# Optimization experiments

Measured on AMD Instinct MI355X. Metric: run time of the kernel, lower is better.

Reference implementation:

```python
import jax, jax.numpy as jnp
import numpy as np
import math

D_MODEL = 1024
N_HEADS = 16
D_HEAD = D_MODEL // N_HEADS
EPS = 1e-5


def layer_norm(x, w, b):
    mu = jnp.mean(x, axis=-1, keepdims=True)
    var = jnp.mean(jnp.square(x - mu), axis=-1, keepdims=True)
    return (x - mu) * jax.lax.rsqrt(var + EPS) * w + b


def setup_inputs() -> dict:
    key = jax.random.key(0)
    ks = jax.random.split(key, 8)
    b, n, d = 1, 4096, D_MODEL
    s = 0.02
    return {
        "x": jax.random.normal(ks[0], (b, n, d), dtype=jnp.float32),
        "ln1_w": jnp.ones((d,), jnp.float32),
        "ln1_b": jnp.zeros((d,), jnp.float32),
        "ln2_w": jnp.ones((d,), jnp.float32),
        "ln2_b": jnp.zeros((d,), jnp.float32),
        "w_qkv": jax.random.normal(ks[1], (d, 3 * d), jnp.float32) * s,  # [in, out]
        "w_o": jax.random.normal(ks[2], (d, d), jnp.float32) * s,
        "w_ff1": jax.random.normal(ks[3], (d, 4 * d), jnp.float32) * s,
        "b_ff1": jnp.zeros((4 * d,), jnp.float32),
        "w_ff2": jax.random.normal(ks[4], (4 * d, d), jnp.float32) * s,
        "b_ff2": jnp.zeros((d,), jnp.float32),
    }


def reference(x, ln1_w, ln1_b, ln2_w, ln2_b, w_qkv, w_o, w_ff1, b_ff1, w_ff2, b_ff2):
    b, n, d = x.shape
    # --- attention sub-block ---
    h = layer_norm(x, ln1_w, ln1_b)
    qkv = (h @ w_qkv).reshape(b, n, 3, N_HEADS, D_HEAD)
    q, k, v = qkv[:, :, 0], qkv[:, :, 1], qkv[:, :, 2]  # [b, n, h, dh]
    scale = 1.0 / math.sqrt(D_HEAD)
    s = jnp.einsum("bqhd,bkhd->bhqk", q, k) * scale  # materialized [b,h,n,n]
    causal = jnp.tril(jnp.ones((n, n), dtype=bool))
    s = jnp.where(causal, s, -jnp.inf)
    a = jax.nn.softmax(s, axis=-1)
    out = jnp.einsum("bhqk,bkhd->bqhd", a, v).reshape(b, n, d)
    x = x + out @ w_o
    # --- FFN sub-block ---
    h2 = layer_norm(x, ln2_w, ln2_b)
    ff = jax.nn.gelu(h2 @ w_ff1 + b_ff1, approximate=False) @ w_ff2 + b_ff2
    return x + ff
```

## Files before the change

kernel.cpp:

```cpp
#include <hip/hip_runtime.h>
#include <hip/hip_bf16.h>
#include <cstdint>
#include <cstddef>

typedef __attribute__((ext_vector_type(8))) __bf16 bf16x8;
typedef __attribute__((ext_vector_type(4))) __bf16 bf16x4;
typedef __attribute__((ext_vector_type(4))) float f32x4;
typedef __attribute__((ext_vector_type(16))) float f32x16;
typedef __attribute__((ext_vector_type(4))) unsigned int uint4v;

#define MFMA16(a, b, c) __builtin_amdgcn_mfma_f32_16x16x32_bf16(a, b, c, 0, 0, 0)
#define MFMA32(a, b, c) __builtin_amdgcn_mfma_f32_32x32x16_bf16(a, b, c, 0, 0, 0)

__device__ __forceinline__ void gload_lds16(const void* g, void* l) {
  __builtin_amdgcn_global_load_lds(
      (__attribute__((address_space(1))) uint32_t*)g,
      (__attribute__((address_space(3))) uint32_t*)l,
      16, 0, 0);
}

__device__ __forceinline__ unsigned pkbf(float a, float b) {
  unsigned short x = __builtin_bit_cast(unsigned short, (__bf16)a);
  unsigned short y = __builtin_bit_cast(unsigned short, (__bf16)b);
  return (unsigned)x | ((unsigned)y << 16);
}

__global__ __launch_bounds__(256) void transpose_all_kernel(
    const float* __restrict__ w_qkv, __bf16* __restrict__ wqkvT,
    const float* __restrict__ w_o, __bf16* __restrict__ woT,
    const float* __restrict__ w_ff1, __bf16* __restrict__ wff1T,
    const float* __restrict__ w_ff2, __bf16* __restrict__ wff2T) {
  __shared__ float tile[32][33];
  int bid = blockIdx.x;
  const float* in; __bf16* out; int K, N, bx, by;
  if (bid < 3072)      { in = w_qkv; out = wqkvT; K = 1024; N = 3072; bx = bid % 96;  by = bid / 96; }
  else if (bid < 4096) { int b = bid - 3072; in = w_o;   out = woT;   K = 1024; N = 1024; bx = b % 32;  by = b / 32; }
  else if (bid < 8192) { int b = bid - 4096; in = w_ff1; out = wff1T; K = 1024; N = 4096; bx = b % 128; by = b / 128; }
  else                 { int b = bid - 8192; in = w_ff2; out = wff2T; K = 4096; N = 1024; bx = b % 32;  by = b / 32; }
  int tx = threadIdx.x, ty = threadIdx.y;
  int gcol = bx * 32 + tx;
#pragma unroll
  for (int j = 0; j < 4; j++) {
    int grow = by * 32 + ty + j * 8;
    tile[ty + j * 8][tx] = in[(size_t)grow * N + gcol];
  }
  __syncthreads();
#pragma unroll
  for (int j = 0; j < 4; j++) {
    int n = bx * 32 + ty + j * 8;
    out[(size_t)n * K + by * 32 + tx] = (__bf16)tile[tx][ty + j * 8];
  }
}

__global__ __launch_bounds__(256) void ln_kernel(
    const float* __restrict__ x, const float* __restrict__ w,
    const float* __restrict__ b, __bf16* __restrict__ out) {
  int row = blockIdx.x;
  int t = threadIdx.x;
  const float4* xr = (const float4*)(x + (size_t)row * 1024);
  float4 v = xr[t];
  float s = v.x + v.y + v.z + v.w;
  float sq = v.x * v.x + v.y * v.y + v.z * v.z + v.w * v.w;
#pragma unroll
  for (int m = 1; m < 64; m <<= 1) {
    s += __shfl_xor(s, m);
    sq += __shfl_xor(sq, m);
  }
  __shared__ float rs[4], rq[4];
  int wid = t >> 6;
  if ((t & 63) == 0) { rs[wid] = s; rq[wid] = sq; }
  __syncthreads();
  s = rs[0] + rs[1] + rs[2] + rs[3];
  sq = rq[0] + rq[1] + rq[2] + rq[3];
  float mean = s * (1.0f / 1024.0f);
  float var = sq * (1.0f / 1024.0f) - mean * mean;
  float rstd = rsqrtf(var + 1e-5f);
  int c = t * 4;
  float4 wv = ((const float4*)w)[t];
  float4 bv = ((const float4*)b)[t];
  bf16x4 o;
  o[0] = (__bf16)((v.x - mean) * rstd * wv.x + bv.x);
  o[1] = (__bf16)((v.y - mean) * rstd * wv.y + bv.y);
  o[2] = (__bf16)((v.z - mean) * rstd * wv.z + bv.z);
  o[3] = (__bf16)((v.w - mean) * rstd * wv.w + bv.w);
  *(bf16x4*)(out + (size_t)row * 1024 + c) = o;
}

template <int EPI>
__global__ __launch_bounds__(256, 2) void gemm_kernel(
    const __bf16* __restrict__ A, const __bf16* __restrict__ BT,
    int M, int N, int K,
    const float* __restrict__ resid, const float* __restrict__ bias,
    float* __restrict__ outf, __bf16* __restrict__ outb) {
  __shared__ __bf16 lsA[128 * 64];
  __shared__ __bf16 lsB[128 * 64];
  int t = threadIdx.x;
  int m0 = blockIdx.y * 128, n0 = blockIdx.x * 128;
  int wid = t >> 6, lane = t & 63, lo = lane & 15, g = lane >> 4;
  int wr = wid >> 1, wc = wid & 1;
  f32x4 acc[4][4] = {};
  const __bf16* ag = A + (size_t)(m0 + (t >> 3)) * K + (t & 7) * 8;
  const __bf16* bg = BT + (size_t)(n0 + (t >> 3)) * K + (t & 7) * 8;
  for (int k0 = 0; k0 < K; k0 += 64) {
#pragma unroll
    for (int i = 0; i < 4; i++) {
      gload_lds16(ag + (size_t)i * 32 * K + k0, &lsA[i * 2048 + t * 8]);
      gload_lds16(bg + (size_t)i * 32 * K + k0, &lsB[i * 2048 + t * 8]);
    }
    __syncthreads();
#pragma unroll
    for (int kk = 0; kk < 2; kk++) {
      bf16x8 af[4], bfr[4];
#pragma unroll
      for (int mi = 0; mi < 4; mi++)
        af[mi] = *(const bf16x8*)&lsA[(wr * 64 + mi * 16 + lo) * 64 + kk * 32 + g * 8];
#pragma unroll
      for (int ni = 0; ni < 4; ni++)
        bfr[ni] = *(const bf16x8*)&lsB[(wc * 64 + ni * 16 + lo) * 64 + kk * 32 + g * 8];
#pragma unroll
      for (int mi = 0; mi < 4; mi++)
#pragma unroll
        for (int ni = 0; ni < 4; ni++)
          acc[mi][ni] = MFMA16(af[mi], bfr[ni], acc[mi][ni]);
    }
    __syncthreads();
  }
#pragma unroll
  for (int mi = 0; mi < 4; mi++) {
#pragma unroll
    for (int ni = 0; ni < 4; ni++) {
      int col = n0 + wc * 64 + ni * 16 + lo;
      int row0 = m0 + wr * 64 + mi * 16 + g * 4;
#pragma unroll
      for (int r = 0; r < 4; r++) {
        int row = row0 + r;
        float val = acc[mi][ni][r];
        size_t idx = (size_t)row * N + col;
        outf[idx] = resid[idx] + val;
      }
    }
  }
}

template <int EPI>
__global__ __launch_bounds__(512, 2) void gemm256_kernel(
    const __bf16* __restrict__ A, const __bf16* __restrict__ BT,
    int M, int N, int K, int nkc,
    const float* __restrict__ bias, __bf16* __restrict__ outb,
    __bf16* __restrict__ P0, __bf16* __restrict__ P1,
    __bf16* __restrict__ P2, __bf16* __restrict__ P3) {
  __shared__ __bf16 lsA[2][2][128 * 64];
  __shared__ __bf16 lsB[2][2][128 * 64];
  int nbx = N >> 8;
  int nwg = (M >> 8) * nbx;
  int bid = blockIdx.x;
  int swz = (bid & 7) * (nwg >> 3) + (bid >> 3);
  int m0 = (swz / nbx) << 8, n0 = (swz % nbx) << 8;
  int kc = blockIdx.y;
  int kt0 = kc * nkc;
  int t = threadIdx.x;
  int wid = t >> 6, lane = t & 63, lo = lane & 15, g = lane >> 4;
  int wm = wid >> 2, wn = wid & 3;
  int srow = t >> 3, sgrp = t & 7;

  auto stA = [&](int d, int h, int kt) {
#pragma unroll
    for (int i = 0; i < 2; i++) {
      int row = i * 64 + srow;
      int gs = (sgrp ^ (row & 7)) * 8;
      gload_lds16(A + (size_t)(m0 + h * 128 + row) * K + kt * 64 + gs,
                  &lsA[d][h][(i * 512 + t) * 8]);
    }
  };
  auto stB = [&](int d, int h, int kt) {
#pragma unroll
    for (int i = 0; i < 2; i++) {
      int row = i * 64 + srow;
      int gs = (sgrp ^ (row & 7)) * 8;
      gload_lds16(BT + (size_t)(n0 + h * 128 + row) * K + kt * 64 + gs,
                  &lsB[d][h][(i * 512 + t) * 8]);
    }
  };
  auto rdA = [&](int d, int f, int kk) -> bf16x8 {
    int row = (f & 3) * 32 + wm * 16 + lo;
    return *(const bf16x8*)&lsA[d][f >> 2][row * 64 + (((kk * 4 + g) ^ (lo & 7)) * 8)];
  };
  auto rdB = [&](int d, int ni, int kk) -> bf16x8 {
    int row = (ni & 1) * 64 + wn * 16 + lo;
    return *(const bf16x8*)&lsB[d][ni >> 1][row * 64 + (((kk * 4 + g) ^ (lo & 7)) * 8)];
  };

  f32x4 acc[8][4] = {};
  stA(0, 0, kt0); stB(0, 0, kt0); stB(0, 1, kt0); stA(0, 1, kt0);
  asm volatile("s_waitcnt vmcnt(4)" ::: "memory");
  __builtin_amdgcn_s_barrier();

  for (int ki = 0; ki < nkc; ki++) {
    int kt = kt0 + ki;
    int d = ki & 1, nx = d ^ 1;
    bool pf = (ki + 1) < nkc;
    bf16x8 fa[4][2], fb0[2][2], fb1[2][2];
#pragma unroll
    for (int f = 0; f < 4; f++) { fa[f][0] = rdA(d, f, 0); fa[f][1] = rdA(d, f, 1); }
#pragma unroll
    for (int n = 0; n < 2; n++) { fb0[n][0] = rdB(d, n, 0); fb0[n][1] = rdB(d, n, 1); }
    if (pf) { stA(nx, 0, kt + 1); stB(nx, 0, kt + 1); }
    __builtin_amdgcn_s_barrier();
    __builtin_amdgcn_s_setprio(1);
#pragma unroll
    for (int f = 0; f < 4; f++)
#pragma unroll
      for (int n = 0; n < 2; n++) {
        acc[f][n] = MFMA16(fa[f][0], fb0[n][0], acc[f][n]);
        acc[f][n] = MFMA16(fa[f][1], fb0[n][1], acc[f][n]);
      }
    __builtin_amdgcn_s_setprio(0);
    asm volatile("s_waitcnt vmcnt(6)" ::: "memory");
    __builtin_amdgcn_s_barrier();
#pragma unroll
    for (int n = 0; n < 2; n++) { fb1[n][0] = rdB(d, 2 + n, 0); fb1[n][1] = rdB(d, 2 + n, 1); }
    if (pf) stB(nx, 1, kt + 1);
    __builtin_amdgcn_s_barrier();
    __builtin_amdgcn_s_setprio(1);
#pragma unroll
    for (int f = 0; f < 4; f++)
#pragma unroll
      for (int n = 0; n < 2; n++) {
        acc[f][2 + n] = MFMA16(fa[f][0], fb1[n][0], acc[f][2 + n]);
        acc[f][2 + n] = MFMA16(fa[f][1], fb1[n][1], acc[f][2 + n]);
      }
    __builtin_amdgcn_s_setprio(0);
    asm volatile("s_waitcnt vmcnt(6)" ::: "memory");
    __builtin_amdgcn_s_barrier();
#pragma unroll
    for (int f = 0; f < 4; f++) { fa[f][0] = rdA(d, 4 + f, 0); fa[f][1] = rdA(d, 4 + f, 1); }
    if (pf) stA(nx, 1, kt + 1);
    __builtin_amdgcn_s_barrier();
    __builtin_amdgcn_s_setprio(1);
#pragma unroll
    for (int f = 0; f < 4; f++)
#pragma unroll
      for (int n = 0; n < 2; n++) {
        acc[4 + f][2 + n] = MFMA16(fa[f][0], fb1[n][0], acc[4 + f][2 + n]);
        acc[4 + f][2 + n] = MFMA16(fa[f][1], fb1[n][1], acc[4 + f][2 + n]);
      }
    __builtin_amdgcn_s_setprio(0);
    __builtin_amdgcn_s_barrier();
    __builtin_amdgcn_s_setprio(1);
#pragma unroll
    for (int f = 0; f < 4; f++)
#pragma unroll
      for (int n = 0; n < 2; n++) {
        acc[4 + f][n] = MFMA16(fa[f][0], fb0[n][0], acc[4 + f][n]);
        acc[4 + f][n] = MFMA16(fa[f][1], fb0[n][1], acc[4 + f][n]);
      }
    __builtin_amdgcn_s_setprio(0);
    asm volatile("s_waitcnt vmcnt(4)" ::: "memory");
    __builtin_amdgcn_s_barrier();
  }

  __bf16* pk = (EPI == 4) ? ((kc == 0) ? P0 : (kc == 1) ? P1 : (kc == 2) ? P2 : P3)
                          : nullptr;
#pragma unroll
  for (int f = 0; f < 8; f++) {
    int row0 = m0 + (f >> 2) * 128 + (f & 3) * 32 + wm * 16 + g * 4;
#pragma unroll
    for (int ni = 0; ni < 4; ni++) {
      int col = n0 + (ni >> 1) * 128 + (ni & 1) * 64 + wn * 16 + lo;
      if (EPI == 0) {
        int sE = col >> 10, rem = col & 1023, hh = rem >> 6, dd = rem & 63;
        if (sE < 2) {
          float qs = (sE == 0) ? 0.1803368801111204f : 1.0f;
#pragma unroll
          for (int r = 0; r < 4; r++)
            outb[((size_t)(sE * 16 + hh) * 4096 + row0 + r) * 64 + dd] =
                (__bf16)(acc[f][ni][r] * qs);
        } else {
          bf16x4 pk4;
#pragma unroll
          for (int r = 0; r < 4; r++) pk4[r] = (__bf16)acc[f][ni][r];
          *(bf16x4*)&outb[(size_t)32 * 4096 * 64 + ((size_t)(hh * 64 + dd)) * 4096 + row0] = pk4;
        }
      } else if (EPI == 2) {
        float bv = bias[col];
#pragma unroll
        for (int r = 0; r < 4; r++) {
          float vv = acc[f][ni][r] + bv;
          float gg = 0.5f * vv * (1.0f + erff(vv * 0.70710678118f));
          outb[(size_t)(row0 + r) * N + col] = (__bf16)gg;
        }
      } else {
#pragma unroll
        for (int r = 0; r < 4; r++)
          pk[(size_t)(row0 + r) * N + col] = (__bf16)acc[f][ni][r];
      }
    }
  }
}

__global__ __launch_bounds__(256) void ff2_reduce_kernel(
    const __bf16* __restrict__ p0, const __bf16* __restrict__ p1,
    const __bf16* __restrict__ p2, const __bf16* __restrict__ p3,
    const float* __restrict__ x2, const float* __restrict__ bias,
    float* __restrict__ out) {
  size_t i8 = ((size_t)blockIdx.x * 256 + threadIdx.x) * 8;
  bf16x8 a = *(const bf16x8*)&p0[i8];
  bf16x8 b = *(const bf16x8*)&p1[i8];
  bf16x8 c = *(const bf16x8*)&p2[i8];
  bf16x8 d = *(const bf16x8*)&p3[i8];
  int col = (int)(i8 & 1023);
  float4 xa = *(const float4*)&x2[i8];
  float4 xb = *(const float4*)&x2[i8 + 4];
  float4 ba = *(const float4*)&bias[col];
  float4 bb = *(const float4*)&bias[col + 4];
  float4 oa, ob;
  oa.x = xa.x + ba.x + (float)a[0] + (float)b[0] + (float)c[0] + (float)d[0];
  oa.y = xa.y + ba.y + (float)a[1] + (float)b[1] + (float)c[1] + (float)d[1];
  oa.z = xa.z + ba.z + (float)a[2] + (float)b[2] + (float)c[2] + (float)d[2];
  oa.w = xa.w + ba.w + (float)a[3] + (float)b[3] + (float)c[3] + (float)d[3];
  ob.x = xb.x + bb.x + (float)a[4] + (float)b[4] + (float)c[4] + (float)d[4];
  ob.y = xb.y + bb.y + (float)a[5] + (float)b[5] + (float)c[5] + (float)d[5];
  ob.z = xb.z + bb.z + (float)a[6] + (float)b[6] + (float)c[6] + (float)d[6];
  ob.w = xb.w + bb.w + (float)a[7] + (float)b[7] + (float)c[7] + (float)d[7];
  *(float4*)&out[i8] = oa;
  *(float4*)&out[i8 + 4] = ob;
}

__global__ __launch_bounds__(512, 4) void attn_kernel(
    const __bf16* __restrict__ Q, const __bf16* __restrict__ Kb,
    const __bf16* __restrict__ VTb, __bf16* __restrict__ O) {
  constexpr int NSEQ = 4096;
  __shared__ __bf16 lds[2][2][2][64 * 64];
  int orig = blockIdx.x;
  int xcd = orig & 7, rank = orig >> 3;
  int hv = rank >> 5;
  int hd2 = (rank >> 4) & 1;
  int itr = rank & 15;
  int head = xcd * 2 + hd2;
  int it = hv ? itr : (31 - itr);
  int t = threadIdx.x, wid = t >> 6, lane = t & 63;
  int lo = lane & 31, hi = lane >> 5;
  int qsub = wid & 3, kpar = wid >> 2;
  const __bf16* kh = Kb + (size_t)head * NSEQ * 64;
  const __bf16* vth = VTb + (size_t)head * 64 * NSEQ;
  int qlow = it * 128 + qsub * 32;
  int qrow = qlow + lo;
  const __bf16* qh = Q + (size_t)head * NSEQ * 64 + (size_t)qrow * 64;
  bf16x8 bq[4];
#pragma unroll
  for (int c = 0; c < 4; c++) bq[c] = *(const bf16x8*)(qh + c * 16 + hi * 8);

  const unsigned onesu = 0x3F803F80u;
  uint4v onev = {onesu, onesu, onesu, onesu};
  bf16x8 vones = __builtin_bit_cast(bf16x8, onev);

  f32x16 acc0 = {}, acc1 = {};
  f32x16 lacc = {};
  int srow = t >> 3;
  int sgs = ((t & 7) ^ (srow & 7)) * 8;

  auto stage_tile = [&](int d, int par, int kt) {
    gload_lds16(kh + (size_t)(kt * 64 + srow) * 64 + sgs, &lds[d][par][0][t * 8]);
    gload_lds16(vth + (size_t)srow * NSEQ + kt * 64 + sgs, &lds[d][par][1][t * 8]);
  };

  int ns = it + 1;
  stage_tile(0, 0, 0);
  stage_tile(0, 1, 1);
  __syncthreads();
  for (int j = 0; j < ns; j++) {
    int cur = j & 1;
    if (j + 1 < ns) {
      stage_tile(cur ^ 1, 0, 2 * j + 2);
      stage_tile(cur ^ 1, 1, 2 * j + 3);
    }
    int kt = 2 * j + kpar;
    if (kt * 64 <= qlow + 31) {
      const __bf16* lk = lds[cur][kpar][0];
      const __bf16* lvt = lds[cur][kpar][1];
      f32x16 s0 = {}, s1 = {};
      __builtin_amdgcn_s_setprio(1);
#pragma unroll
      for (int c = 0; c < 4; c++) {
        bf16x8 ka0 = *(const bf16x8*)&lk[(size_t)lo * 64 + (((c * 2 + hi) ^ (lo & 7)) * 8)];
        bf16x8 ka1 = *(const bf16x8*)&lk[(size_t)(32 + lo) * 64 + (((c * 2 + hi) ^ (lo & 7)) * 8)];
        s0 = MFMA32(ka0, bq[c], s0);
        s1 = MFMA32(ka1, bq[c], s1);
      }
      __builtin_amdgcn_s_setprio(0);
      if (kt * 64 + 63 > qlow) {
#pragma unroll
        for (int i = 0; i < 16; i++) {
          int key0 = kt * 64 + (i & 3) + 8 * (i >> 2) + 4 * hi;
          if (key0 > qrow) s0[i] = -3.0e38f;
          if (key0 + 32 > qrow) s1[i] = -3.0e38f;
        }
      }
#pragma unroll
      for (int i = 0; i < 16; i++) {
        s0[i] = exp2f(s0[i]);
        s1[i] = exp2f(s1[i]);
      }
      uint4v pw[4];
#pragma unroll
      for (int b = 0; b < 2; b++) {
        int off = b * 8;
        unsigned a0 = pkbf(s0[off + 0], s0[off + 1]);
        unsigned a1 = pkbf(s0[off + 2], s0[off + 3]);
        unsigned b0 = pkbf(s0[off + 4], s0[off + 5]);
        unsigned b1 = pkbf(s0[off + 6], s0[off + 7]);
        asm("v_permlane32_swap_b32 %0, %1" : "+v"(a0), "+v"(b0));
        asm("v_permlane32_swap_b32 %0, %1" : "+v"(a1), "+v"(b1));
        pw[b][0] = a0; pw[b][1] = a1; pw[b][2] = b0; pw[b][3] = b1;
        unsigned c0 = pkbf(s1[off + 0], s1[off + 1]);
        unsigned c1 = pkbf(s1[off + 2], s1[off + 3]);
        unsigned d0 = pkbf(s1[off + 4], s1[off + 5]);
        unsigned d1 = pkbf(s1[off + 6], s1[off + 7]);
        asm("v_permlane32_swap_b32 %0, %1" : "+v"(c0), "+v"(d0));
        asm("v_permlane32_swap_b32 %0, %1" : "+v"(c1), "+v"(d1));
        pw[2 + b][0] = c0; pw[2 + b][1] = c1; pw[2 + b][2] = d0; pw[2 + b][3] = d1;
      }
      __builtin_amdgcn_s_setprio(1);
#pragma unroll
      for (int b = 0; b < 4; b++) {
        bf16x8 pf = __builtin_bit_cast(bf16x8, pw[b]);
        bf16x8 va0 = *(const bf16x8*)&lvt[(size_t)lo * 64 + (((b * 2 + hi) ^ (lo & 7)) * 8)];
        bf16x8 va1 = *(const bf16x8*)&lvt[(size_t)(32 + lo) * 64 + (((b * 2 + hi) ^ (lo & 7)) * 8)];
        acc0 = MFMA32(va0, pf, acc0);
        acc1 = MFMA32(va1, pf, acc1);
        lacc = MFMA32(vones, pf, lacc);
      }
      __builtin_amdgcn_s_setprio(0);
    }
    __syncthreads();
  }
  float* fl = (float*)lds;
  float* lbuf = fl;
  float* ab = fl + 256;
  __bf16* bounce = (__bf16*)(fl + 256 + 9216);
  if (kpar == 1) {
    lbuf[qsub * 64 + lane] = lacc[0];
    int base = (qsub * 64 + lane) * 36;
#pragma unroll
    for (int k2 = 0; k2 < 16; k2 += 4) {
      float4 v0; v0.x = acc0[k2]; v0.y = acc0[k2 + 1]; v0.z = acc0[k2 + 2]; v0.w = acc0[k2 + 3];
      *(float4*)&ab[base + k2] = v0;
      float4 v1; v1.x = acc1[k2]; v1.y = acc1[k2 + 1]; v1.z = acc1[k2 + 2]; v1.w = acc1[k2 + 3];
      *(float4*)&ab[base + 16 + k2] = v1;
    }
  }
  __syncthreads();
  if (kpar == 0) {
    float lsum = lacc[0] + lbuf[qsub * 64 + lane];
    float linv = 1.0f / lsum;
    int base = (qsub * 64 + lane) * 36;
    f32x16 b0, b1;
#pragma unroll
    for (int k2 = 0; k2 < 16; k2 += 4) {
      float4 v0 = *(float4*)&ab[base + k2];
      b0[k2] = v0.x; b0[k2 + 1] = v0.y; b0[k2 + 2] = v0.z; b0[k2 + 3] = v0.w;
      float4 v1 = *(float4*)&ab[base + 16 + k2];
      b1[k2] = v1.x; b1[k2 + 1] = v1.y; b1[k2 + 2] = v1.z; b1[k2 + 3] = v1.w;
    }
    __bf16* region = bounce + qsub * 2048;
#pragma unroll
    for (int dt = 0; dt < 2; dt++) {
#pragma unroll
      for (int rp = 0; rp < 8; rp++) {
        int r = rp * 2;
        float a0 = dt ? acc1[r] : acc0[r], a1 = dt ? acc1[r + 1] : acc0[r + 1];
        float c0 = dt ? b1[r] : b0[r], c1 = dt ? b1[r + 1] : b0[r + 1];
        float e0 = (a0 + c0) * linv;
        float e1 = (a1 + c1) * linv;
        int d = dt * 32 + (r & 3) + 8 * (r >> 2) + 4 * hi;
        int bytecol = d * 2;
        int g16 = bytecol >> 4, rem16 = bytecol & 15;
        *(unsigned*)((char*)region + lo * 128 + ((g16 ^ (lo & 7)) * 16 + rem16)) = pkbf(e0, e1);
      }
    }
#pragma unroll
    for (int j2 = 0; j2 < 4; j2++) {
      int idx = j2 * 64 + lane;
      int row = idx >> 3, g = idx & 7;
      bf16x8 v = *(const bf16x8*)((char*)region + row * 128 + ((g ^ (row & 7)) * 16));
      *(bf16x8*)&O[(size_t)(it * 128 + qsub * 32 + row) * 1024 + head * 64 + g * 8] = v;
    }
  }
}

extern "C" void kernel_launch(void* const* d_in, const int* in_sizes, int n_in,
                              void* d_out, int out_size, void* d_ws, size_t ws_size,
                              hipStream_t stream) {
  const float* x = (const float*)d_in[0];
  const float* ln1_w = (const float*)d_in[1];
  const float* ln1_b = (const float*)d_in[2];
  const float* ln2_w = (const float*)d_in[3];
  const float* ln2_b = (const float*)d_in[4];
  const float* w_qkv = (const float*)d_in[5];
  const float* w_o = (const float*)d_in[6];
  const float* w_ff1 = (const float*)d_in[7];
  const float* b_ff1 = (const float*)d_in[8];
  const float* w_ff2 = (const float*)d_in[9];
  const float* b_ff2 = (const float*)d_in[10];
  float* out = (float*)d_out;

  const size_t D = 1024, NT = 4096;
  __bf16* wqkvT = (__bf16*)d_ws;
  __bf16* woT = wqkvT + 3072 * D;
  __bf16* wff1T = woT + D * D;
  __bf16* wff2T = wff1T + 4096 * D;
  __bf16* hbuf = wff2T + D * 4096;
  __bf16* qkvb = hbuf + NT * D;
  __bf16* attnb = qkvb + 3 * NT * D;
  __bf16* a1 = qkvb;
  float* x2 = (float*)(attnb + NT * D);
  __bf16* p0 = (__bf16*)d_ws;
  __bf16* p1 = p0 + NT * D;
  __bf16* p2 = hbuf;
  __bf16* p3 = (__bf16*)(x2 + NT * D);

  dim3 tb(32, 8);
  transpose_all_kernel<<<12288, tb, 0, stream>>>(w_qkv, wqkvT, w_o, woT,
                                                 w_ff1, wff1T, w_ff2, wff2T);

  ln_kernel<<<4096, 256, 0, stream>>>(x, ln1_w, ln1_b, hbuf);
  gemm256_kernel<0><<<192, 512, 0, stream>>>(hbuf, wqkvT, 4096, 3072, 1024, 16,
                                             nullptr, qkvb, nullptr, nullptr, nullptr, nullptr);
  attn_kernel<<<512, 512, 0, stream>>>(
      qkvb, qkvb + 16 * NT * 64, qkvb + 32 * NT * 64, attnb);
  gemm_kernel<1><<<dim3(1024 / 128, 4096 / 128), 256, 0, stream>>>(
      attnb, woT, 4096, 1024, 1024, x, nullptr, x2, nullptr);
  ln_kernel<<<4096, 256, 0, stream>>>(x2, ln2_w, ln2_b, hbuf);
  gemm256_kernel<2><<<256, 512, 0, stream>>>(hbuf, wff1T, 4096, 4096, 1024, 16,
                                             b_ff1, a1, nullptr, nullptr, nullptr, nullptr);
  gemm256_kernel<4><<<dim3(64, 4), 512, 0, stream>>>(a1, wff2T, 4096, 1024, 4096, 16,
                                                     nullptr, nullptr, p0, p1, p2, p3);
  ff2_reduce_kernel<<<2048, 256, 0, stream>>>(p0, p1, p2, p3, x2, b_ff2, out);
}
```

Before: 247.8 us.

## Split-K the output projection, fuse residual with LN2, single-buffer attention LDS

The output-projection GEMM is split into two K-halves that write bf16 partials, so it launches twice as many workgroups. A new kernel sums the partials with the residual and applies LayerNorm 2, replacing the separate GEMM epilogue and ln_kernel pass. The attention kernel drops the double-buffered K/V staging for a single buffer loaded synchronously each iteration and stages the kpar=1 partial output as bf16, which cuts LDS use and raises the occupancy hint to 6. The trade-offs are lost prefetch overlap in attention, extra bf16 rounding of the partial sums, and an extra partial-buffer round trip through memory.

```diff
diff --git a/kernel.cpp b/kernel.cpp
--- a/kernel.cpp
+++ b/kernel.cpp
@@ -86,22 +86,21 @@
   *(bf16x4*)(out + (size_t)row * 1024 + c) = o;
 }
 
-template <int EPI>
-__global__ __launch_bounds__(256, 2) void gemm_kernel(
+__global__ __launch_bounds__(256, 2) void gemm_splitk128_kernel(
     const __bf16* __restrict__ A, const __bf16* __restrict__ BT,
-    int M, int N, int K,
-    const float* __restrict__ resid, const float* __restrict__ bias,
-    float* __restrict__ outf, __bf16* __restrict__ outb) {
+    int M, int N, int K, int kchunk, __bf16* __restrict__ P) {
   __shared__ __bf16 lsA[128 * 64];
   __shared__ __bf16 lsB[128 * 64];
   int t = threadIdx.x;
   int m0 = blockIdx.y * 128, n0 = blockIdx.x * 128;
+  int kbase = blockIdx.z * kchunk;
+  __bf16* pout = P + (size_t)blockIdx.z * M * N;
   int wid = t >> 6, lane = t & 63, lo = lane & 15, g = lane >> 4;
   int wr = wid >> 1, wc = wid & 1;
   f32x4 acc[4][4] = {};
   const __bf16* ag = A + (size_t)(m0 + (t >> 3)) * K + (t & 7) * 8;
   const __bf16* bg = BT + (size_t)(n0 + (t >> 3)) * K + (t & 7) * 8;
-  for (int k0 = 0; k0 < K; k0 += 64) {
+  for (int k0 = kbase; k0 < kbase + kchunk; k0 += 64) {
 #pragma unroll
     for (int i = 0; i < 4; i++) {
       gload_lds16(ag + (size_t)i * 32 * K + k0, &lsA[i * 2048 + t * 8]);
@@ -132,14 +131,52 @@
       int col = n0 + wc * 64 + ni * 16 + lo;
       int row0 = m0 + wr * 64 + mi * 16 + g * 4;
 #pragma unroll
-      for (int r = 0; r < 4; r++) {
-        int row = row0 + r;
-        float val = acc[mi][ni][r];
-        size_t idx = (size_t)row * N + col;
-        outf[idx] = resid[idx] + val;
-      }
-    }
-  }
+      for (int r = 0; r < 4; r++)
+        pout[(size_t)(row0 + r) * N + col] = (__bf16)acc[mi][ni][r];
+    }
+  }
+}
+
+__global__ __launch_bounds__(256) void out_reduce_ln_kernel(
+    const __bf16* __restrict__ p0, const __bf16* __restrict__ p1,
+    const float* __restrict__ x, const float* __restrict__ w,
+    const float* __restrict__ b, float* __restrict__ x2,
+    __bf16* __restrict__ h) {
+  int row = blockIdx.x, t = threadIdx.x;
+  size_t base = (size_t)row * 1024 + t * 4;
+  bf16x4 a = *(const bf16x4*)&p0[base];
+  bf16x4 b4 = *(const bf16x4*)&p1[base];
+  float4 xv = *(const float4*)&x[base];
+  float4 v;
+  v.x = xv.x + (float)a[0] + (float)b4[0];
+  v.y = xv.y + (float)a[1] + (float)b4[1];
+  v.z = xv.z + (float)a[2] + (float)b4[2];
+  v.w = xv.w + (float)a[3] + (float)b4[3];
+  *(float4*)&x2[base] = v;
+  float s = v.x + v.y + v.z + v.w;
+  float sq = v.x * v.x + v.y * v.y + v.z * v.z + v.w * v.w;
+#pragma unroll
+  for (int m = 1; m < 64; m <<= 1) {
+    s += __shfl_xor(s, m);
+    sq += __shfl_xor(sq, m);
+  }
+  __shared__ float rs[4], rq[4];
+  int wid = t >> 6;
+  if ((t & 63) == 0) { rs[wid] = s; rq[wid] = sq; }
+  __syncthreads();
+  s = rs[0] + rs[1] + rs[2] + rs[3];
+  sq = rq[0] + rq[1] + rq[2] + rq[3];
+  float mean = s * (1.0f / 1024.0f);
+  float var = sq * (1.0f / 1024.0f) - mean * mean;
+  float rstd = rsqrtf(var + 1e-5f);
+  float4 wv = ((const float4*)w)[t];
+  float4 bv = ((const float4*)b)[t];
+  bf16x4 o;
+  o[0] = (__bf16)((v.x - mean) * rstd * wv.x + bv.x);
+  o[1] = (__bf16)((v.y - mean) * rstd * wv.y + bv.y);
+  o[2] = (__bf16)((v.z - mean) * rstd * wv.z + bv.z);
+  o[3] = (__bf16)((v.w - mean) * rstd * wv.w + bv.w);
+  *(bf16x4*)&h[base] = o;
 }
 
 template <int EPI>
@@ -326,11 +363,11 @@
   *(float4*)&out[i8 + 4] = ob;
 }
 
-__global__ __launch_bounds__(512, 4) void attn_kernel(
+__global__ __launch_bounds__(512, 6) void attn_kernel(
     const __bf16* __restrict__ Q, const __bf16* __restrict__ Kb,
     const __bf16* __restrict__ VTb, __bf16* __restrict__ O) {
   constexpr int NSEQ = 4096;
-  __shared__ __bf16 lds[2][2][2][64 * 64];
+  __shared__ __bf16 lds[2][2][64 * 64];
   int orig = blockIdx.x;
   int xcd = orig & 7, rank = orig >> 3;
   int hv = rank >> 5;
@@ -345,6 +382,7 @@
   const __bf16* vth = VTb + (size_t)head * 64 * NSEQ;
   int qlow = it * 128 + qsub * 32;
   int qrow = qlow + lo;
+  int lastk = (qlow + 31) >> 6;
   const __bf16* qh = Q + (size_t)head * NSEQ * 64 + (size_t)qrow * 64;
   bf16x8 bq[4];
 #pragma unroll
@@ -359,31 +397,30 @@
   int srow = t >> 3;
   int sgs = ((t & 7) ^ (srow & 7)) * 8;
 
-  auto stage_tile = [&](int d, int par, int kt) {
-    gload_lds16(kh + (size_t)(kt * 64 + srow) * 64 + sgs, &lds[d][par][0][t * 8]);
-    gload_lds16(vth + (size_t)srow * NSEQ + kt * 64 + sgs, &lds[d][par][1][t * 8]);
-  };
-
-  int ns = it + 1;
-  stage_tile(0, 0, 0);
-  stage_tile(0, 1, 1);
-  __syncthreads();
-  for (int j = 0; j < ns; j++) {
-    int cur = j & 1;
-    if (j + 1 < ns) {
-      stage_tile(cur ^ 1, 0, 2 * j + 2);
-      stage_tile(cur ^ 1, 1, 2 * j + 3);
-    }
-    int kt = 2 * j + kpar;
-    if (kt * 64 <= qlow + 31) {
-      const __bf16* lk = lds[cur][kpar][0];
-      const __bf16* lvt = lds[cur][kpar][1];
+  int off[4];
+#pragma unroll
+  for (int c = 0; c < 4; c++) off[c] = lo * 64 + (((c * 2 + hi) ^ (lo & 7)) * 8);
+  const __bf16* lk = &lds[kpar][0][0];
+  const __bf16* lvt = &lds[kpar][1][0];
+  const __bf16* khs = kh + srow * 64 + sgs;
+  const __bf16* vts = vth + (size_t)srow * NSEQ + sgs;
+
+  int ns2 = it + 1;
+  for (int j = 0; j < ns2; j++) {
+    int k0 = 2 * j;
+    gload_lds16(khs + (size_t)k0 * 4096, &lds[0][0][t * 8]);
+    gload_lds16(vts + k0 * 64, &lds[0][1][t * 8]);
+    gload_lds16(khs + (size_t)(k0 + 1) * 4096, &lds[1][0][t * 8]);
+    gload_lds16(vts + (k0 + 1) * 64, &lds[1][1][t * 8]);
+    __syncthreads();
+    int kt = k0 + kpar;
+    if (kt <= lastk) {
       f32x16 s0 = {}, s1 = {};
       __builtin_amdgcn_s_setprio(1);
 #pragma unroll
       for (int c = 0; c < 4; c++) {
-        bf16x8 ka0 = *(const bf16x8*)&lk[(size_t)lo * 64 + (((c * 2 + hi) ^ (lo & 7)) * 8)];
-        bf16x8 ka1 = *(const bf16x8*)&lk[(size_t)(32 + lo) * 64 + (((c * 2 + hi) ^ (lo & 7)) * 8)];
+        bf16x8 ka0 = *(const bf16x8*)&lk[off[c]];
+        bf16x8 ka1 = *(const bf16x8*)&lk[2048 + off[c]];
         s0 = MFMA32(ka0, bq[c], s0);
         s1 = MFMA32(ka1, bq[c], s1);
       }
@@ -404,28 +441,29 @@
       uint4v pw[4];
 #pragma unroll
       for (int b = 0; b < 2; b++) {
-        int off = b * 8;
-        unsigned a0 = pkbf(s0[off + 0], s0[off + 1]);
-        unsigned a1 = pkbf(s0[off + 2], s0[off + 3]);
-        unsigned b0 = pkbf(s0[off + 4], s0[off + 5]);
-        unsigned b1 = pkbf(s0[off + 6], s0[off + 7]);
+        int off2 = b * 8;
+        unsigned a0 = pkbf(s0[off2 + 0], s0[off2 + 1]);
+        unsigned a1 = pkbf(s0[off2 + 2], s0[off2 + 3]);
+        unsigned b0 = pkbf(s0[off2 + 4], s0[off2 + 5]);
+        unsigned b1 = pkbf(s0[off2 + 6], s0[off2 + 7]);
         asm("v_permlane32_swap_b32 %0, %1" : "+v"(a0), "+v"(b0));
         asm("v_permlane32_swap_b32 %0, %1" : "+v"(a1), "+v"(b1));
         pw[b][0] = a0; pw[b][1] = a1; pw[b][2] = b0; pw[b][3] = b1;
-        unsigned c0 = pkbf(s1[off + 0], s1[off + 1]);
-        unsigned c1 = pkbf(s1[off + 2], s1[off + 3]);
-        unsigned d0 = pkbf(s1[off + 4], s1[off + 5]);
-        unsigned d1 = pkbf(s1[off + 6], s1[off + 7]);
+        unsigned c0 = pkbf(s1[off2 + 0], s1[off2 + 1]);
+        unsigned c1 = pkbf(s1[off2 + 2], s1[off2 + 3]);
+        unsigned d0 = pkbf(s1[off2 + 4], s1[off2 + 5]);
+        unsigned d1 = pkbf(s1[off2 + 6], s1[off2 + 7]);
         asm("v_permlane32_swap_b32 %0, %1" : "+v"(c0), "+v"(d0));
         asm("v_permlane32_swap_b32 %0, %1" : "+v"(c1), "+v"(d1));
-        pw[2 + b][0] = c0; pw[2 + b][1] = c1; pw[2 + b][2] = d0; pw[2 + b][3] = d1;
+        pw[2 + b][0] = c0; pw[2 + b][1] = c1; pw[2 + b][2] = d0;
+        pw[2 + b][3] = d1;
       }
       __builtin_amdgcn_s_setprio(1);
 #pragma unroll
       for (int b = 0; b < 4; b++) {
         bf16x8 pf = __builtin_bit_cast(bf16x8, pw[b]);
-        bf16x8 va0 = *(const bf16x8*)&lvt[(size_t)lo * 64 + (((b * 2 + hi) ^ (lo & 7)) * 8)];
-        bf16x8 va1 = *(const bf16x8*)&lvt[(size_t)(32 + lo) * 64 + (((b * 2 + hi) ^ (lo & 7)) * 8)];
+        bf16x8 va0 = *(const bf16x8*)&lvt[off[b]];
+        bf16x8 va1 = *(const bf16x8*)&lvt[2048 + off[b]];
         acc0 = MFMA32(va0, pf, acc0);
         acc1 = MFMA32(va1, pf, acc1);
         lacc = MFMA32(vones, pf, lacc);
@@ -434,48 +472,45 @@
     }
     __syncthreads();
   }
+
   float* fl = (float*)lds;
   float* lbuf = fl;
-  float* ab = fl + 256;
-  __bf16* bounce = (__bf16*)(fl + 256 + 9216);
+  __bf16* bounce = (__bf16*)(fl + 256);
+  __bf16* region = bounce + qsub * 2048;
   if (kpar == 1) {
     lbuf[qsub * 64 + lane] = lacc[0];
-    int base = (qsub * 64 + lane) * 36;
-#pragma unroll
-    for (int k2 = 0; k2 < 16; k2 += 4) {
-      float4 v0; v0.x = acc0[k2]; v0.y = acc0[k2 + 1]; v0.z = acc0[k2 + 2]; v0.w = acc0[k2 + 3];
-      *(float4*)&ab[base + k2] = v0;
-      float4 v1; v1.x = acc1[k2]; v1.y = acc1[k2 + 1]; v1.z = acc1[k2 + 2]; v1.w = acc1[k2 + 3];
-      *(float4*)&ab[base + 16 + k2] = v1;
-    }
-  }
-  __syncthreads();
-  if (kpar == 0) {
-    float lsum = lacc[0] + lbuf[qsub * 64 + lane];
-    float linv = 1.0f / lsum;
-    int base = (qsub * 64 + lane) * 36;
-    f32x16 b0, b1;
-#pragma unroll
-    for (int k2 = 0; k2 < 16; k2 += 4) {
-      float4 v0 = *(float4*)&ab[base + k2];
-      b0[k2] = v0.x; b0[k2 + 1] = v0.y; b0[k2 + 2] = v0.z; b0[k2 + 3] = v0.w;
-      float4 v1 = *(float4*)&ab[base + 16 + k2];
-      b1[k2] = v1.x; b1[k2 + 1] = v1.y; b1[k2 + 2] = v1.z; b1[k2 + 3] = v1.w;
-    }
-    __bf16* region = bounce + qsub * 2048;
 #pragma unroll
     for (int dt = 0; dt < 2; dt++) {
 #pragma unroll
       for (int rp = 0; rp < 8; rp++) {
         int r = rp * 2;
-        float a0 = dt ? acc1[r] : acc0[r], a1 = dt ? acc1[r + 1] : acc0[r + 1];
-        float c0 = dt ? b1[r] : b0[r], c1 = dt ? b1[r + 1] : b0[r + 1];
-        float e0 = (a0 + c0) * linv;
-        float e1 = (a1 + c1) * linv;
+        float e0 = dt ? acc1[r] : acc0[r];
+        float e1 = dt ? acc1[r + 1] : acc0[r + 1];
         int d = dt * 32 + (r & 3) + 8 * (r >> 2) + 4 * hi;
         int bytecol = d * 2;
         int g16 = bytecol >> 4, rem16 = bytecol & 15;
         *(unsigned*)((char*)region + lo * 128 + ((g16 ^ (lo & 7)) * 16 + rem16)) = pkbf(e0, e1);
+      }
+    }
+  }
+  __syncthreads();
+  if (kpar == 0) {
+    float linv = 1.0f / (lacc[0] + lbuf[qsub * 64 + lane]);
+#pragma unroll
+    for (int dt = 0; dt < 2; dt++) {
+#pragma unroll
+      for (int rp = 0; rp < 8; rp++) {
+        int r = rp * 2;
+        int d = dt * 32 + (r & 3) + 8 * (r >> 2) + 4 * hi;
+        int bytecol = d * 2;
+        int g16 = bytecol >> 4, rem16 = bytecol & 15;
+        unsigned* addr = (unsigned*)((char*)region + lo * 128 + ((g16 ^ (lo & 7)) * 16 + rem16));
+        unsigned u = *addr;
+        float plo = (float)__builtin_bit_cast(__bf16, (unsigned short)(u & 0xffff));
+        float phi = (float)__builtin_bit_cast(__bf16, (unsigned short)(u >> 16));
+        float e0 = ((dt ? acc1[r] : acc0[r]) + plo) * linv;
+        float e1 = ((dt ? acc1[r + 1] : acc0[r + 1]) + phi) * linv;
+        *addr = pkbf(e0, e1);
       }
     }
 #pragma unroll
@@ -518,6 +553,8 @@
   __bf16* p1 = p0 + NT * D;
   __bf16* p2 = hbuf;
   __bf16* p3 = (__bf16*)(x2 + NT * D);
+  __bf16* pA = qkvb;
+  __bf16* pB = pA + NT * D;
 
   dim3 tb(32, 8);
   transpose_all_kernel<<<12288, tb, 0, stream>>>(w_qkv, wqkvT, w_o, woT,
@@ -528,9 +565,9 @@
                                              nullptr, qkvb, nullptr, nullptr, nullptr, nullptr);
   attn_kernel<<<512, 512, 0, stream>>>(
       qkvb, qkvb + 16 * NT * 64, qkvb + 32 * NT * 64, attnb);
-  gemm_kernel<1><<<dim3(1024 / 128, 4096 / 128), 256, 0, stream>>>(
-      attnb, woT, 4096, 1024, 1024, x, nullptr, x2, nullptr);
-  ln_kernel<<<4096, 256, 0, stream>>>(x2, ln2_w, ln2_b, hbuf);
+  gemm_splitk128_kernel<<<dim3(8, 32, 2), 256, 0, stream>>>(
+      attnb, woT, 4096, 1024, 1024, 512, pA);
+  out_reduce_ln_kernel<<<4096, 256, 0, stream>>>(pA, pB, x, ln2_w, ln2_b, x2, hbuf);
   gemm256_kernel<2><<<256, 512, 0, stream>>>(hbuf, wff1T, 4096, 4096, 1024, 16,
                                              b_ff1, a1, nullptr, nullptr, nullptr, nullptr);
   gemm256_kernel<4><<<dim3(64, 4), 512, 0, stream>>>(a1, wff2T, 4096, 1024, 4096, 16,
```

After: 539.9 us. 118% more time.
